# Performance work log

Hardware: AMD Instinct MI355X
Metric: run time of the kernel (lower is better)

## Reference

```python
import jax, jax.numpy as jnp
import numpy as np

B, S, D, H, CLIP = 4, 1024, 1024, 16, 64
DH = D // H

def setup_inputs() -> dict:
    key = jax.random.key(0)
    ks = jax.random.split(key, 10)
    sc = 1.0 / np.sqrt(D)
    return {
        "queries": jax.random.normal(ks[0], (B, S, D), jnp.float32),
        "keys": jax.random.normal(ks[1], (B, S, D), jnp.float32),
        "values": jax.random.normal(ks[2], (B, S, D), jnp.float32),
        "valid_lens": jax.random.randint(ks[3], (B,), 0, S),
        "Wq": jax.random.normal(ks[4], (D, D), jnp.float32) * sc,
        "Wk": jax.random.normal(ks[5], (D, D), jnp.float32) * sc,
        "Wv": jax.random.normal(ks[6], (D, D), jnp.float32) * sc,
        "Wo": jax.random.normal(ks[7], (D, D), jnp.float32) * sc,
        "rpr_k": jax.random.normal(ks[8], (2 * CLIP + 1, DH), jnp.float32),
        "rpr_v": jax.random.normal(ks[9], (2 * CLIP + 1, DH), jnp.float32),
    }

def reference(queries, keys, values, valid_lens, Wq, Wk, Wv, Wo, rpr_k, rpr_v):
    # project and split heads: [B,S,D] -> [B,H,S,DH]
    def split(x, W):
        return (x @ W).reshape(B, S, H, DH).transpose(0, 2, 1, 3)
    q = split(queries, Wq)
    k = split(keys, Wk)
    v = split(values, Wv)
    # relative position indices [S,S] in [0, 2*CLIP]
    dist = jnp.arange(S)[None, :] - jnp.arange(S)[:, None]
    dist = jnp.clip(dist, -CLIP, CLIP) + CLIP
    pos_k = rpr_k[dist]  # [S,S,DH]
    pos_v = rpr_v[dist]  # [S,S,DH]
    # content scores + relative-position key bias
    scores = jnp.einsum('bhqd,bhkd->bhqk', q, k)
    scores = scores + jnp.einsum('bhqd,qkd->bhqk', q, pos_k)
    scores = scores / jnp.sqrt(jnp.asarray(DH, q.dtype))
    # masked softmax: positions >= valid_len set to -1e6 (matches torch code)
    key_mask = jnp.arange(S)[None, None, None, :] < valid_lens[:, None, None, None]
    scores = jnp.where(key_mask, scores, jnp.asarray(-1e6, scores.dtype))
    attn = jax.nn.softmax(scores, axis=-1)  # [B,H,S,S]
    # value aggregation + relative-position value bias
    out = jnp.einsum('bhqk,bhkd->bhqd', attn, v)
    out = out + jnp.einsum('bhqk,qkd->bhqd', attn, pos_v)
    out = out.transpose(0, 2, 1, 3).reshape(B, S, D)
    return out @ Wo
```

## Files before the change

kernel.cpp:

```cpp
#include <hip/hip_runtime.h>
#include <stdint.h>
#include <math.h>

#define BB 4
#define SS 1024
#define DD 1024
#define HH 16
#define DHH 64
#define NCLIP 64
#define NCC 129
#define NCP 160
#define QRSTR 148
#define M0F 20.0f

typedef __bf16 bf16;
typedef __bf16 bf16x8 __attribute__((ext_vector_type(8)));
typedef float f32x4 __attribute__((ext_vector_type(4)));

__device__ __forceinline__ void gload_lds16(const void* g, void* l) {
  __builtin_amdgcn_global_load_lds((const __attribute__((address_space(1))) void*)g,
                                   (__attribute__((address_space(3))) void*)l, 16, 0, 0);
}

struct TpArgs { const float* w[4]; bf16* wt[4]; };
__global__ __launch_bounds__(256) void transpose_pack_w(TpArgs args) {
  const float* __restrict__ W = args.w[blockIdx.z];
  bf16* __restrict__ Wt = args.wt[blockIdx.z];
  __shared__ float tile[32][33];
  int tx = threadIdx.x, ty = threadIdx.y;
  int n0 = blockIdx.x * 32, k0 = blockIdx.y * 32;
#pragma unroll
  for (int i = 0; i < 4; i++)
    tile[ty + i * 8][tx] = W[(size_t)(k0 + ty + i * 8) * DD + n0 + tx];
  __syncthreads();
#pragma unroll
  for (int i = 0; i < 4; i++)
    Wt[(size_t)(n0 + ty + i * 8) * DD + k0 + tx] = (bf16)tile[tx][ty + i * 8];
}

struct CvtArgs { const float* in[3]; bf16* out[3]; int skip[3]; };
__global__ __launch_bounds__(256) void f32_to_bf16_3(CvtArgs args, const int* __restrict__ vlens) {
  const int z = blockIdx.z;
  if (args.skip[z]) {
    int row0 = (blockIdx.x * 2) & 1023;
    int b = (blockIdx.x * 2) >> 10;
    int vl = vlens[b];
    if (vl > 0 && row0 >= vl) return;
  }
  const float* __restrict__ in = args.in[z];
  bf16* __restrict__ out = args.out[z];
  size_t i = ((size_t)blockIdx.x * 256 + threadIdx.x) * 8;
  f32x4 v0 = *(const f32x4*)(in + i);
  f32x4 v1 = *(const f32x4*)(in + i + 4);
  bf16x8 o;
#pragma unroll
  for (int j = 0; j < 4; j++) { o[j] = (bf16)v0[j]; o[j + 4] = (bf16)v1[j]; }
  *(bf16x8*)(out + i) = o;
}

struct GemmArgs { const bf16* a[3]; const bf16* bt[3]; void* c[3]; float sc[3]; int skip[3]; };
template <bool SPLIT>
__global__ __launch_bounds__(256) void gemm128(GemmArgs args, const int* __restrict__ vlens) {
  const int z = blockIdx.z;
  const int m0 = blockIdx.y * 128, n0 = blockIdx.x * 128;
  if (args.skip[z]) {
    int vl = vlens[m0 >> 10];
    if (vl > 0 && (m0 & 1023) >= vl) return;
  }
  const bf16* __restrict__ A  = args.a[z];
  const bf16* __restrict__ Bt = args.bt[z];
  void* __restrict__ Cv = args.c[z];
  const float scale = args.sc[z];
  __shared__ __align__(16) bf16 As[128][32];
  __shared__ __align__(16) bf16 Bs[128][32];
  const int tid = threadIdx.x, lane = tid & 63, wv = tid >> 6;
  const int wr = wv >> 1, wc = wv & 1;
  const int l15 = lane & 15, l4 = lane >> 4;
  const int srow = lane >> 2, scol = (lane & 3) * 8;
  f32x4 z4 = {0.f, 0.f, 0.f, 0.f};
  f32x4 acc[4][4];
#pragma unroll
  for (int i = 0; i < 4; i++)
#pragma unroll
    for (int j = 0; j < 4; j++) acc[i][j] = z4;

  for (int k0 = 0; k0 < DD; k0 += 32) {
    gload_lds16(A  + (size_t)(m0 + wv * 16 + srow) * DD + k0 + scol,      &As[wv * 16][0]);
    gload_lds16(A  + (size_t)(m0 + 64 + wv * 16 + srow) * DD + k0 + scol, &As[64 + wv * 16][0]);
    gload_lds16(Bt + (size_t)(n0 + wv * 16 + srow) * DD + k0 + scol,      &Bs[wv * 16][0]);
    gload_lds16(Bt + (size_t)(n0 + 64 + wv * 16 + srow) * DD + k0 + scol, &Bs[64 + wv * 16][0]);
    __syncthreads();
    bf16x8 af[4], bfv[4];
#pragma unroll
    for (int i = 0; i < 4; i++) {
      af[i]  = *(const bf16x8*)&As[wr * 64 + i * 16 + l15][l4 * 8];
      bfv[i] = *(const bf16x8*)&Bs[wc * 64 + i * 16 + l15][l4 * 8];
    }
#pragma unroll
    for (int mi = 0; mi < 4; mi++)
#pragma unroll
      for (int ni = 0; ni < 4; ni++)
        acc[mi][ni] = __builtin_amdgcn_mfma_f32_16x16x32_bf16(af[mi], bfv[ni], acc[mi][ni], 0, 0, 0);
    __syncthreads();
  }
#pragma unroll
  for (int mi = 0; mi < 4; mi++)
#pragma unroll
    for (int ni = 0; ni < 4; ni++)
#pragma unroll
      for (int r = 0; r < 4; r++) {
        int m = m0 + wr * 64 + mi * 16 + l4 * 4 + r;
        int n = n0 + wc * 64 + ni * 16 + l15;
        float val = acc[mi][ni][r] * scale;
        if (SPLIT) {
          ((bf16*)Cv)[((((size_t)(m >> 10) * HH + (n >> 6)) * SS) + (m & 1023)) * DHH + (n & 63)] =
              (bf16)val;
        } else {
          ((float*)Cv)[(size_t)m * DD + n] = val;
        }
      }
}

__global__ __launch_bounds__(256) void gemm_bf16_final(const bf16* __restrict__ A,
                                                       const bf16* __restrict__ Bt,
                                                       float* __restrict__ C) {
  __shared__ __align__(16) bf16 As[64][32];
  __shared__ __align__(16) bf16 Bs[128][32];
  const int tid = threadIdx.x, lane = tid & 63, wv = tid >> 6;
  const int l15 = lane & 15, l4 = lane >> 4;
  const int m0 = blockIdx.y * 64, n0 = blockIdx.x * 128;
  const int srow = lane >> 2, scol = (lane & 3) * 8;
  f32x4 z4 = {0.f, 0.f, 0.f, 0.f};
  f32x4 acc[4][2];
#pragma unroll
  for (int i = 0; i < 4; i++) { acc[i][0] = z4; acc[i][1] = z4; }

  for (int k0 = 0; k0 < DD; k0 += 32) {
    gload_lds16(A + (size_t)(m0 + wv * 16 + srow) * DD + k0 + scol, &As[wv * 16][0]);
    gload_lds16(Bt + (size_t)(n0 + wv * 32 + srow) * DD + k0 + scol, &Bs[wv * 32][0]);
    gload_lds16(Bt + (size_t)(n0 + wv * 32 + 16 + srow) * DD + k0 + scol, &Bs[wv * 32 + 16][0]);
    __syncthreads();
    bf16x8 af[4], bfv[2];
#pragma unroll
    for (int i = 0; i < 4; i++) af[i] = *(const bf16x8*)&As[i * 16 + l15][l4 * 8];
#pragma unroll
    for (int i = 0; i < 2; i++) bfv[i] = *(const bf16x8*)&Bs[wv * 32 + i * 16 + l15][l4 * 8];
#pragma unroll
    for (int mi = 0; mi < 4; mi++)
#pragma unroll
      for (int ni = 0; ni < 2; ni++)
        acc[mi][ni] = __builtin_amdgcn_mfma_f32_16x16x32_bf16(af[mi], bfv[ni], acc[mi][ni], 0, 0, 0);
    __syncthreads();
  }
#pragma unroll
  for (int mi = 0; mi < 4; mi++)
#pragma unroll
    for (int ni = 0; ni < 2; ni++)
#pragma unroll
      for (int r = 0; r < 4; r++) {
        int m = m0 + mi * 16 + l4 * 4 + r;
        int n = n0 + wv * 32 + ni * 16 + l15;
        C[(size_t)m * DD + n] = acc[mi][ni][r];
      }
}

__global__ __launch_bounds__(256) void vh_transpose(const bf16* __restrict__ Vh,
                                                    bf16* __restrict__ VhT,
                                                    const int* __restrict__ vlens) {
  __shared__ bf16 til[64][65];
  int bh = blockIdx.y;
  int s0 = blockIdx.x * 64;
  int vl = vlens[bh >> 4];
  if (vl > 0 && s0 >= vl + 32) return;
  const bf16* src = Vh + (size_t)bh * SS * DHH + (size_t)s0 * DHH;
  for (int i = threadIdx.x; i < 64 * 64; i += 256) {
    int r = i >> 6, cc = i & 63;
    til[r][cc] = src[(size_t)r * DHH + cc];
  }
  __syncthreads();
  bf16* dst = VhT + (size_t)bh * DHH * SS + s0;
  for (int i = threadIdx.x; i < 64 * 64; i += 256) {
    int d = i >> 6, cc = i & 63;
    dst[(size_t)d * SS + cc] = til[cc][d];
  }
}

__global__ void prep_tables(const float* __restrict__ rpr_v, const float* __restrict__ rpr_k,
                            bf16* __restrict__ rvT, bf16* __restrict__ rkP) {
  int i = blockIdx.x * 256 + threadIdx.x;
  if (i < DHH * NCP) {
    int d = i / NCP, c = i - d * NCP;
    rvT[i] = (c < NCC) ? (bf16)rpr_v[(size_t)c * DHH + d] : (bf16)0.f;
  }
  if (i < 144 * 64) {
    rkP[i] = (i < NCC * DHH) ? (bf16)rpr_k[i] : (bf16)0.f;
  }
}

__global__ __launch_bounds__(256, 3) void attn_mfma(
    const bf16* __restrict__ Qh, const bf16* __restrict__ Kh, const bf16* __restrict__ VhT,
    const bf16* __restrict__ rkP, const int* __restrict__ valid_lens,
    const bf16* __restrict__ rvT, bf16* __restrict__ Obh) {
  __shared__ __align__(16) bf16 Ks[32][64];
  __shared__ __align__(16) bf16 Vs[64][32];
  __shared__ __align__(16) char arena[4][10240];
  const int tid = threadIdx.x, lane = tid & 63, w = tid >> 6;
  const int l15 = lane & 15, l4 = lane >> 4;
  const int b = blockIdx.z, h = blockIdx.y, bh = b * HH + h;
  const int q0 = blockIdx.x * 64 + w * 16;
  const int vlen = valid_lens[b];
  const float mval = (vlen == 0) ? 0.f : -30000.f;
  char* base = arena[w];
  bf16* QRs = (bf16*)base;
  _Float16* SBand = (_Float16*)(base + 4736);
  bf16* Pl = (bf16*)(base + 8832);

  const bf16* Qbase = Qh + ((size_t)bh * SS + q0) * DHH;
  bf16x8 qa0 = *(const bf16x8*)(Qbase + (size_t)l15 * DHH + l4 * 8);
  bf16x8 qa1 = *(const bf16x8*)(Qbase + (size_t)l15 * DHH + 32 + l4 * 8);
  const bf16* Kbase = Kh + (size_t)bh * SS * DHH;
  const bf16* Vbase = VhT + (size_t)bh * DHH * SS;
  f32x4 z = {0.f, 0.f, 0.f, 0.f};

#pragma unroll
  for (int ni = 0; ni < 9; ni++) {
    const bf16* rp = rkP + (size_t)(ni * 16 + l15) * DHH + l4 * 8;
    bf16x8 b0 = *(const bf16x8*)(rp);
    bf16x8 b1 = *(const bf16x8*)(rp + 32);
    f32x4 acc = __builtin_amdgcn_mfma_f32_16x16x32_bf16(qa0, b0, z, 0, 0, 0);
    acc = __builtin_amdgcn_mfma_f32_16x16x32_bf16(qa1, b1, acc, 0, 0, 0);
#pragma unroll
    for (int r = 0; r < 4; r++)
      QRs[(l4 * 4 + r) * QRSTR + ni * 16 + l15] = (bf16)acc[r];
  }
  {
    _Float16 ninf = (_Float16)(-65504.f);
    for (int i = lane; i < 16 * 128; i += 64) SBand[i] = ninf;
  }

  float biasLo[4], biasHi[4];
#pragma unroll
  for (int r = 0; r < 4; r++) {
    biasLo[r] = (float)QRs[(l4 * 4 + r) * QRSTR + 0];
    biasHi[r] = (float)QRs[(l4 * 4 + r) * QRSTR + 128];
  }

  float l_lane[4], slo[4], shi[4];
#pragma unroll
  for (int r = 0; r < 4; r++) { l_lane[r] = 0.f; slo[r] = 0.f; shi[r] = 0.f; }
  f32x4 acco[4];
#pragma unroll
  for (int i = 0; i < 4; i++) acco[i] = z;

  const int ksw0 = (l4 ^ (l15 & 7)) * 8;
  const int ksw1 = ((l4 + 4) ^ (l15 & 7)) * 8;
  const int vsw  = (l4 ^ (l15 & 3)) * 8;
  const int krow = w * 8 + (lane >> 3);
  const int kch  = ((lane & 7) ^ (krow & 7)) * 8;
  const int vd   = w * 16 + (lane >> 2);
  const int vch  = ((lane & 3) ^ (vd & 3)) * 8;

  const int kfb = (vlen > 0) ? (vlen & ~31) : 0;
  const int kte = (vlen > 0) ? ((vlen + 31) & ~31) : SS;
  int bs = q0 - 94; bs = (bs < 0) ? 0 : ((bs + 31) & ~31);
  int be = (q0 + 110) & ~31; if (be > SS) be = SS;

  for (int ks = 0; ks < kte; ks += 32) {
    gload_lds16(Kbase + (size_t)(ks + krow) * DHH + kch, &Ks[w * 8][0]);
    gload_lds16(Vbase + (size_t)vd * SS + ks + vch, &Vs[w * 16][0]);
    __syncthreads();
    bf16x8 kf00 = *(const bf16x8*)&Ks[l15][ksw0];
    bf16x8 kf01 = *(const bf16x8*)&Ks[l15][ksw1];
    bf16x8 kf10 = *(const bf16x8*)&Ks[16 + l15][ksw0];
    bf16x8 kf11 = *(const bf16x8*)&Ks[16 + l15][ksw1];
    f32x4 a0 = __builtin_amdgcn_mfma_f32_16x16x32_bf16(qa0, kf00, z, 0, 0, 0);
    a0 = __builtin_amdgcn_mfma_f32_16x16x32_bf16(qa1, kf01, a0, 0, 0, 0);
    f32x4 a1 = __builtin_amdgcn_mfma_f32_16x16x32_bf16(qa0, kf10, z, 0, 0, 0);
    a1 = __builtin_amdgcn_mfma_f32_16x16x32_bf16(qa1, kf11, a1, 0, 0, 0);

    if (ks >= kfb) {
      const int rel = ks - q0;
      const int mode = (rel <= -95) ? 0 : (rel >= 79) ? 1 : 2;
#pragma unroll
      for (int sub = 0; sub < 2; sub++) {
        const f32x4 a = sub ? a1 : a0;
        const int kg = ks + sub * 16 + l15;
        const bool msk = (kg >= vlen);
        if (mode == 0) {
#pragma unroll
          for (int r = 0; r < 4; r++) {
            float s = msk ? mval : (a[r] + biasLo[r]);
            float p = __expf(s - M0F);
            l_lane[r] += p; slo[r] += p;
            Pl[(l4 * 4 + r) * 40 + sub * 16 + l15] = (bf16)p;
          }
        } else if (mode == 1) {
#pragma unroll
          for (int r = 0; r < 4; r++) {
            float s = msk ? mval : (a[r] + biasHi[r]);
            float p = __expf(s - M0F);
            l_lane[r] += p; shi[r] += p;
            Pl[(l4 * 4 + r) * 40 + sub * 16 + l15] = (bf16)p;
          }
        } else {
#pragma unroll
          for (int r = 0; r < 4; r++) {
            const int qloc = l4 * 4 + r;
            int dlt = kg - q0 - qloc;
            int c = (dlt < -NCLIP ? -NCLIP : (dlt > NCLIP ? NCLIP : dlt)) + NCLIP;
            float s = a[r] + (float)QRs[qloc * QRSTR + c];
            if (msk) s = mval;
            if (dlt > -64 && dlt < 64) SBand[qloc * 128 + dlt + 63] = (_Float16)s;
            float p = __expf(s - M0F);
            l_lane[r] += p;
            slo[r] += (dlt <= -64) ? p : 0.f;
            shi[r] += (dlt >= 64) ? p : 0.f;
            Pl[qloc * 40 + sub * 16 + l15] = (bf16)p;
          }
        }
      }
    } else if (ks < bs) {
#pragma unroll
      for (int sub = 0; sub < 2; sub++) {
        const f32x4 a = sub ? a1 : a0;
#pragma unroll
        for (int r = 0; r < 4; r++) {
          float p = __expf(a[r] + biasLo[r] - M0F);
          l_lane[r] += p; slo[r] += p;
          Pl[(l4 * 4 + r) * 40 + sub * 16 + l15] = (bf16)p;
        }
      }
    } else if (ks < be) {
#pragma unroll
      for (int sub = 0; sub < 2; sub++) {
        const f32x4 a = sub ? a1 : a0;
        const int kg = ks + sub * 16 + l15;
#pragma unroll
        for (int r = 0; r < 4; r++) {
          const int qloc = l4 * 4 + r;
          int dlt = kg - q0 - qloc;
          int c = (dlt < -NCLIP ? -NCLIP : (dlt > NCLIP ? NCLIP : dlt)) + NCLIP;
          float s = a[r] + (float)QRs[qloc * QRSTR + c];
          if (dlt > -64 && dlt < 64) SBand[qloc * 128 + dlt + 63] = (_Float16)s;
          float p = __expf(s - M0F);
          l_lane[r] += p;
          slo[r] += (dlt <= -64) ? p : 0.f;
          shi[r] += (dlt >= 64) ? p : 0.f;
          Pl[qloc * 40 + sub * 16 + l15] = (bf16)p;
        }
      }
    } else {
#pragma unroll
      for (int sub = 0; sub < 2; sub++) {
        const f32x4 a = sub ? a1 : a0;
#pragma unroll
        for (int r = 0; r < 4; r++) {
          float p = __expf(a[r] + biasHi[r] - M0F);
          l_lane[r] += p; shi[r] += p;
          Pl[(l4 * 4 + r) * 40 + sub * 16 + l15] = (bf16)p;
        }
      }
    }

    bf16x8 pa = *(const bf16x8*)&Pl[l15 * 40 + l4 * 8];
    acco[0] = __builtin_amdgcn_mfma_f32_16x16x32_bf16(pa, *(const bf16x8*)&Vs[l15][vsw], acco[0], 0, 0, 0);
    acco[1] = __builtin_amdgcn_mfma_f32_16x16x32_bf16(pa, *(const bf16x8*)&Vs[16 + l15][vsw], acco[1], 0, 0, 0);
    acco[2] = __builtin_amdgcn_mfma_f32_16x16x32_bf16(pa, *(const bf16x8*)&Vs[32 + l15][vsw], acco[2], 0, 0, 0);
    acco[3] = __builtin_amdgcn_mfma_f32_16x16x32_bf16(pa, *(const bf16x8*)&Vs[48 + l15][vsw], acco[3], 0, 0, 0);
    __syncthreads();
  }

  float* li_s   = (float*)(base + 8832);
  float* a0_s   = (float*)(base + 8896);
  float* a128_s = (float*)(base + 8960);
  float li_r[4];
#pragma unroll
  for (int r = 0; r < 4; r++) {
    const int qloc = l4 * 4 + r;
    float lt = l_lane[r], so = slo[r], sh = shi[r];
    lt += __shfl_xor(lt, 1, 64); so += __shfl_xor(so, 1, 64); sh += __shfl_xor(sh, 1, 64);
    lt += __shfl_xor(lt, 2, 64); so += __shfl_xor(so, 2, 64); sh += __shfl_xor(sh, 2, 64);
    lt += __shfl_xor(lt, 4, 64); so += __shfl_xor(so, 4, 64); sh += __shfl_xor(sh, 4, 64);
    lt += __shfl_xor(lt, 8, 64); so += __shfl_xor(so, 8, 64); sh += __shfl_xor(sh, 8, 64);
    float li = 1.f / lt;
    li_r[r] = li;
    if (l15 == 0) { li_s[qloc] = li; a0_s[qloc] = so * li; a128_s[qloc] = sh * li; }
  }
  bf16* AWs = (bf16*)base;
  for (int row = 0; row < 16; row++) {
    float li = li_s[row], a0 = a0_s[row], a128 = a128_s[row];
#pragma unroll
    for (int j = 0; j < 3; j++) {
      int c = lane + 64 * j;
      if (c < 160) {
        float val;
        if (c == 0) val = a0;
        else if (c == 128) val = a128;
        else if (c < 128) val = __expf((float)SBand[row * 128 + c - 1] - M0F) * li;
        else val = 0.f;
        AWs[row * 168 + c] = (bf16)val;
      }
    }
  }
  f32x4 acc2[4];
#pragma unroll
  for (int i = 0; i < 4; i++) acc2[i] = z;
#pragma unroll
  for (int kk = 0; kk < 5; kk++) {
    bf16x8 af = *(const bf16x8*)&AWs[l15 * 168 + kk * 32 + l4 * 8];
#pragma unroll
    for (int ni = 0; ni < 4; ni++) {
      bf16x8 bv = *(const bf16x8*)(rvT + (size_t)(ni * 16 + l15) * NCP + kk * 32 + l4 * 8);
      acc2[ni] = __builtin_amdgcn_mfma_f32_16x16x32_bf16(af, bv, acc2[ni], 0, 0, 0);
    }
  }
#pragma unroll
  for (int ni = 0; ni < 4; ni++)
#pragma unroll
    for (int r = 0; r < 4; r++) {
      int qg = q0 + l4 * 4 + r;
      Obh[((size_t)b * SS + qg) * DD + h * DHH + ni * 16 + l15] =
          (bf16)(acco[ni][r] * li_r[r] + acc2[ni][r]);
    }
}

extern "C" void kernel_launch(void* const* d_in, const int* in_sizes, int n_in,
                              void* d_out, int out_size, void* d_ws, size_t ws_size,
                              hipStream_t stream) {
  (void)in_sizes; (void)n_in; (void)out_size; (void)ws_size;
  const float* queries = (const float*)d_in[0];
  const float* keys    = (const float*)d_in[1];
  const float* values  = (const float*)d_in[2];
  const int*   vlens   = (const int*)d_in[3];
  const float* Wq = (const float*)d_in[4];
  const float* Wk = (const float*)d_in[5];
  const float* Wv = (const float*)d_in[6];
  const float* Wo = (const float*)d_in[7];
  const float* rpr_k = (const float*)d_in[8];
  const float* rpr_v = (const float*)d_in[9];

  char* ws = (char*)d_ws;
  const size_t MB = 1024 * 1024;
  bf16* Wtq  = (bf16*)(ws + 0 * MB);
  bf16* Wtk  = (bf16*)(ws + 2 * MB);
  bf16* Wtv  = (bf16*)(ws + 4 * MB);
  bf16* Wto  = (bf16*)(ws + 6 * MB);
  bf16* Qh   = (bf16*)(ws + 8 * MB);
  bf16* Kh   = (bf16*)(ws + 16 * MB);
  bf16* Vh   = (bf16*)(ws + 24 * MB);
  bf16* VhT  = (bf16*)(ws + 32 * MB);
  bf16* Qb   = (bf16*)(ws + 40 * MB);
  bf16* Kb   = (bf16*)(ws + 48 * MB);
  bf16* Vb   = (bf16*)(ws + 56 * MB);
  bf16* Obh  = (bf16*)(ws + 64 * MB);
  bf16* rvT  = (bf16*)(ws + 72 * MB);
  bf16* rkP  = (bf16*)(ws + 73 * MB);

  TpArgs tp; tp.w[0] = Wq; tp.w[1] = Wk; tp.w[2] = Wv; tp.w[3] = Wo;
  tp.wt[0] = Wtq; tp.wt[1] = Wtk; tp.wt[2] = Wtv; tp.wt[3] = Wto;
  transpose_pack_w<<<dim3(32, 32, 4), dim3(32, 8), 0, stream>>>(tp);

  CvtArgs cv; cv.in[0] = queries; cv.in[1] = keys; cv.in[2] = values;
  cv.out[0] = Qb; cv.out[1] = Kb; cv.out[2] = Vb;
  cv.skip[0] = 0; cv.skip[1] = 1; cv.skip[2] = 1;
  f32_to_bf16_3<<<dim3(2048, 1, 3), 256, 0, stream>>>(cv, vlens);

  GemmArgs gp;
  gp.a[0] = Qb; gp.a[1] = Kb; gp.a[2] = Vb;
  gp.bt[0] = Wtq; gp.bt[1] = Wtk; gp.bt[2] = Wtv;
  gp.c[0] = (void*)Qh; gp.c[1] = (void*)Kh; gp.c[2] = (void*)Vh;
  gp.sc[0] = 0.125f; gp.sc[1] = 1.0f; gp.sc[2] = 1.0f;
  gp.skip[0] = 0; gp.skip[1] = 1; gp.skip[2] = 1;
  gemm128<true><<<dim3(8, 32, 3), 256, 0, stream>>>(gp, vlens);

  vh_transpose<<<dim3(16, 64), 256, 0, stream>>>(Vh, VhT, vlens);
  prep_tables<<<dim3(40), 256, 0, stream>>>(rpr_v, rpr_k, rvT, rkP);
  attn_mfma<<<dim3(16, HH, BB), 256, 0, stream>>>(Qh, Kh, VhT, rkP, vlens, rvT, Obh);
  gemm_bf16_final<<<dim3(8, 64), 256, 0, stream>>>(Obh, Wto, (float*)d_out);
}
```

Before: 114.5 us.

## Double-buffer K tiles in LDS and read V fragments directly from global

Double-buffers the K tile in shared memory: the next 32-row tile is prefetched with global_load_lds while the current one feeds the QK MFMAs, which removes one barrier per iteration. V no longer goes through LDS; each lane loads its bf16x8 V fragment straight from global (L1/L2) memory right before the PV MFMAs. This trims LDS traffic and synchronisation, but V loads now sit on the critical path with no latency hiding, and the single remaining barrier has to cover the async K prefetch.

```diff
diff --git a/kernel.cpp b/kernel.cpp
--- a/kernel.cpp
+++ b/kernel.cpp
@@ -201,8 +201,7 @@
     const bf16* __restrict__ Qh, const bf16* __restrict__ Kh, const bf16* __restrict__ VhT,
     const bf16* __restrict__ rkP, const int* __restrict__ valid_lens,
     const bf16* __restrict__ rvT, bf16* __restrict__ Obh) {
-  __shared__ __align__(16) bf16 Ks[32][64];
-  __shared__ __align__(16) bf16 Vs[64][32];
+  __shared__ __align__(16) bf16 Ks[2][32][64];
   __shared__ __align__(16) char arena[4][10240];
   const int tid = threadIdx.x, lane = tid & 63, w = tid >> 6;
   const int l15 = lane & 15, l4 = lane >> 4;
@@ -252,27 +251,28 @@
 #pragma unroll
   for (int i = 0; i < 4; i++) acco[i] = z;
 
+  const int krow = w * 8 + (lane >> 3);
+  const int kch  = ((lane & 7) ^ (krow & 7)) * 8;
   const int ksw0 = (l4 ^ (l15 & 7)) * 8;
   const int ksw1 = ((l4 + 4) ^ (l15 & 7)) * 8;
-  const int vsw  = (l4 ^ (l15 & 3)) * 8;
-  const int krow = w * 8 + (lane >> 3);
-  const int kch  = ((lane & 7) ^ (krow & 7)) * 8;
-  const int vd   = w * 16 + (lane >> 2);
-  const int vch  = ((lane & 3) ^ (vd & 3)) * 8;
 
   const int kfb = (vlen > 0) ? (vlen & ~31) : 0;
   const int kte = (vlen > 0) ? ((vlen + 31) & ~31) : SS;
   int bs = q0 - 94; bs = (bs < 0) ? 0 : ((bs + 31) & ~31);
   int be = (q0 + 110) & ~31; if (be > SS) be = SS;
 
+  gload_lds16(Kbase + (size_t)krow * DHH + kch, &Ks[0][w * 8][0]);
+  __syncthreads();
+
+  int cur = 0;
   for (int ks = 0; ks < kte; ks += 32) {
-    gload_lds16(Kbase + (size_t)(ks + krow) * DHH + kch, &Ks[w * 8][0]);
-    gload_lds16(Vbase + (size_t)vd * SS + ks + vch, &Vs[w * 16][0]);
-    __syncthreads();
-    bf16x8 kf00 = *(const bf16x8*)&Ks[l15][ksw0];
-    bf16x8 kf01 = *(const bf16x8*)&Ks[l15][ksw1];
-    bf16x8 kf10 = *(const bf16x8*)&Ks[16 + l15][ksw0];
-    bf16x8 kf11 = *(const bf16x8*)&Ks[16 + l15][ksw1];
+    if (ks + 32 < kte)
+      gload_lds16(Kbase + (size_t)(ks + 32 + krow) * DHH + kch, &Ks[cur ^ 1][w * 8][0]);
+
+    bf16x8 kf00 = *(const bf16x8*)&Ks[cur][l15][ksw0];
+    bf16x8 kf01 = *(const bf16x8*)&Ks[cur][l15][ksw1];
+    bf16x8 kf10 = *(const bf16x8*)&Ks[cur][16 + l15][ksw0];
+    bf16x8 kf11 = *(const bf16x8*)&Ks[cur][16 + l15][ksw1];
     f32x4 a0 = __builtin_amdgcn_mfma_f32_16x16x32_bf16(qa0, kf00, z, 0, 0, 0);
     a0 = __builtin_amdgcn_mfma_f32_16x16x32_bf16(qa1, kf01, a0, 0, 0, 0);
     f32x4 a1 = __builtin_amdgcn_mfma_f32_16x16x32_bf16(qa0, kf10, z, 0, 0, 0);
@@ -363,11 +363,13 @@
     }
 
     bf16x8 pa = *(const bf16x8*)&Pl[l15 * 40 + l4 * 8];
-    acco[0] = __builtin_amdgcn_mfma_f32_16x16x32_bf16(pa, *(const bf16x8*)&Vs[l15][vsw], acco[0], 0, 0, 0);
-    acco[1] = __builtin_amdgcn_mfma_f32_16x16x32_bf16(pa, *(const bf16x8*)&Vs[16 + l15][vsw], acco[1], 0, 0, 0);
-    acco[2] = __builtin_amdgcn_mfma_f32_16x16x32_bf16(pa, *(const bf16x8*)&Vs[32 + l15][vsw], acco[2], 0, 0, 0);
-    acco[3] = __builtin_amdgcn_mfma_f32_16x16x32_bf16(pa, *(const bf16x8*)&Vs[48 + l15][vsw], acco[3], 0, 0, 0);
+    const bf16* vp = Vbase + (size_t)l15 * SS + ks + l4 * 8;
+    acco[0] = __builtin_amdgcn_mfma_f32_16x16x32_bf16(pa, *(const bf16x8*)(vp), acco[0], 0, 0, 0);
+    acco[1] = __builtin_amdgcn_mfma_f32_16x16x32_bf16(pa, *(const bf16x8*)(vp + (size_t)16 * SS), acco[1], 0, 0, 0);
+    acco[2] = __builtin_amdgcn_mfma_f32_16x16x32_bf16(pa, *(const bf16x8*)(vp + (size_t)32 * SS), acco[2], 0, 0, 0);
+    acco[3] = __builtin_amdgcn_mfma_f32_16x16x32_bf16(pa, *(const bf16x8*)(vp + (size_t)48 * SS), acco[3], 0, 0, 0);
     __syncthreads();
+    cur ^= 1;
   }
 
   float* li_s   = (float*)(base + 8832);
```

After: 120.1 us. +4.9%, slower.
